# Kernel optimization log

Hardware: AMD Instinct MI355X
Metric: run time of the kernel (lower is better)

## Reference

```python
import jax, jax.numpy as jnp
import numpy as np
from jax import lax

H = 64            # GRU hidden size
NUM_LAYERS = 4
EPS = 1e-5        # BatchNorm eps
NEG_SLOPE = 0.1   # LeakyReLU slope


def setup_inputs() -> dict:
    key = jax.random.key(0)
    ks = jax.random.split(key, 24)
    B, T, D = 4096, 34, 180

    def u(k, shape, fan):
        s = 1.0 / np.sqrt(fan)
        return jax.random.uniform(k, shape, jnp.float32, -s, s)

    inp = {
        "poses": jax.random.normal(ks[0], (B, T, D), jnp.float32),
        # pre_conv: Conv1d(180,16,3) -> BN(16) -> Conv1d(16,8,3) -> BN(8) -> Conv1d(8,8,3)
        "conv1_w": u(ks[1], (16, D, 3), D * 3),
        "conv1_b": u(ks[2], (16,), D * 3),
        "bn1_g": jnp.ones((16,), jnp.float32),
        "bn1_b": jnp.zeros((16,), jnp.float32),
        "conv2_w": u(ks[3], (8, 16, 3), 16 * 3),
        "conv2_b": u(ks[4], (8,), 16 * 3),
        "bn2_g": jnp.ones((8,), jnp.float32),
        "bn2_b": jnp.zeros((8,), jnp.float32),
        "conv3_w": u(ks[5], (8, 8, 3), 8 * 3),
        "conv3_b": u(ks[6], (8,), 8 * 3),
        # GRU layer 0: input 8 -> hidden 64
        "gru0_w_ih": u(ks[7], (3 * H, 8), H),
        # GRU layers 1..3: input 64 -> hidden 64 (stacked)
        "gru_w_ih": u(ks[8], (NUM_LAYERS - 1, 3 * H, H), H),
        "gru_w_hh": u(ks[9], (NUM_LAYERS, 3 * H, H), H),
        "gru_b_ih": u(ks[10], (NUM_LAYERS, 3 * H), H),
        "gru_b_hh": u(ks[11], (NUM_LAYERS, 3 * H), H),
        "out_w": u(ks[12], (1, H), H),
        "out_b": u(ks[13], (1,), H),
        "out2_w": u(ks[14], (1, T - 6), T - 6),
        "out2_b": u(ks[15], (1,), T - 6),
    }
    return inp


def _conv1d(x, w, b):
    # x: [B, C_in, L], w: [C_out, C_in, K] -> [B, C_out, L-K+1]
    y = lax.conv_general_dilated(x, w, (1,), 'VALID',
                                 dimension_numbers=('NCH', 'OIH', 'NCH'))
    return y + b[None, :, None]


def _bn_train(x, g, b):
    # training-mode BatchNorm1d over (batch, length) per channel; x: [B, C, L]
    m = jnp.mean(x, axis=(0, 2), keepdims=True)
    v = jnp.mean(jnp.square(x - m), axis=(0, 2), keepdims=True)  # biased var
    return (x - m) * jax.lax.rsqrt(v + EPS) * g[None, :, None] + b[None, :, None]


def _leaky(x):
    return jnp.where(x >= 0, x, NEG_SLOPE * x)


def _gru_layer(x_tbh, w_ih, w_hh, b_ih, b_hh):
    # x_tbh: [T, B, D_in]; returns outputs [T, B, H]
    xg = jnp.einsum('tbi,gi->tbg', x_tbh, w_ih) + b_ih  # [T, B, 3H]

    def step(h, xg_t):
        hg = h @ w_hh.T + b_hh
        i_r, i_z, i_n = jnp.split(xg_t, 3, axis=-1)
        h_r, h_z, h_n = jnp.split(hg, 3, axis=-1)
        r = jax.nn.sigmoid(i_r + h_r)
        z = jax.nn.sigmoid(i_z + h_z)
        n = jnp.tanh(i_n + r * h_n)
        h_new = n - n * z + z * h  # == (1-z)*n + z*h
        return h_new, h_new

    B = x_tbh.shape[1]
    h0 = jnp.zeros((B, H), x_tbh.dtype)
    _, ys = lax.scan(step, h0, xg)
    return ys


def reference(poses, conv1_w, conv1_b, bn1_g, bn1_b, conv2_w, conv2_b,
              bn2_g, bn2_b, conv3_w, conv3_b, gru0_w_ih, gru_w_ih,
              gru_w_hh, gru_b_ih, gru_b_hh, out_w, out_b, out2_w, out2_b):
    x = jnp.transpose(poses, (0, 2, 1))          # [B, D, T]
    x = _leaky(_bn_train(_conv1d(x, conv1_w, conv1_b), bn1_g, bn1_b))
    x = _leaky(_bn_train(_conv1d(x, conv2_w, conv2_b), bn2_g, bn2_b))
    x = _conv1d(x, conv3_w, conv3_b)             # [B, 8, T-6]
    feat = jnp.transpose(x, (2, 0, 1))           # [T', B, 8] time-major

    out = _gru_layer(feat, gru0_w_ih, gru_w_hh[0], gru_b_ih[0], gru_b_hh[0])
    for i in range(1, NUM_LAYERS):
        out = _gru_layer(out, gru_w_ih[i - 1], gru_w_hh[i], gru_b_ih[i], gru_b_hh[i])

    out = jnp.transpose(out, (1, 0, 2))          # [B, T', H]
    y = jnp.einsum('bth,oh->bto', out, out_w)[..., 0] + out_b[0]  # [B, T']
    y = y @ out2_w[0] + out2_b[0]                # [B]
    return jax.nn.sigmoid(y)[:, None]            # [B, 1]
```

## Files before the change

kernel.cpp:

```cpp
#include <hip/hip_runtime.h>

typedef unsigned short u16;
typedef __attribute__((ext_vector_type(8))) short bf16x8;
typedef __attribute__((ext_vector_type(4))) short bf16x4;
typedef __attribute__((ext_vector_type(4))) float f32x4;

#define TP 28
#define NB 4096
#define L2E 1.4426950408889634f

__device__ __forceinline__ u16 f2bf(float x) {
  union { float f; unsigned u; } v; v.f = x;
  unsigned u = v.u;
  return (u16)((u + 0x7fffu + ((u >> 16) & 1u)) >> 16);
}
__device__ __forceinline__ float bf2f(u16 h) {
  union { unsigned u; float f; } v; v.u = ((unsigned)h) << 16; return v.f;
}
__device__ __forceinline__ float rcp_(float x) {
  float r;
  asm("v_rcp_f32 %0, %1" : "=v"(r) : "v"(x));
  return r;
}
__device__ __forceinline__ float exp2_(float x) {
  float r;
  asm("v_exp_f32 %0, %1" : "=v"(r) : "v"(x));
  return r;
}
__device__ __forceinline__ float sigm2(float x) { return rcp_(1.0f + exp2_(-x)); }
__device__ __forceinline__ float tanh2(float x) { return 1.0f - 2.0f * rcp_(1.0f + exp2_(x)); }
__device__ __forceinline__ float sigm(float x) { return rcp_(1.0f + __expf(-x)); }
__device__ __forceinline__ float leaky(float x) { return x >= 0.0f ? x : 0.1f * x; }
__device__ __forceinline__ f32x4 mfma16(bf16x8 a, bf16x8 b, f32x4 c) {
  return __builtin_amdgcn_mfma_f32_16x16x32_bf16(a, b, c, 0, 0, 0);
}
__device__ __forceinline__ bf16x8 pack8s(float4 a, float4 b, float s) {
  bf16x8 f;
  f[0] = (short)f2bf(a.x * s); f[1] = (short)f2bf(a.y * s);
  f[2] = (short)f2bf(a.z * s); f[3] = (short)f2bf(a.w * s);
  f[4] = (short)f2bf(b.x * s); f[5] = (short)f2bf(b.y * s);
  f[6] = (short)f2bf(b.z * s); f[7] = (short)f2bf(b.w * s);
  return f;
}
__device__ __forceinline__ bf16x8 ldfrag8s(const float* p, float s) {
  float4 u0 = *(const float4*)p;
  float4 u1 = *(const float4*)(p + 4);
  return pack8s(u0, u1, s);
}

__global__ __launch_bounds__(512, 4) void k_conv1(
    const float* __restrict__ poses, const float* __restrict__ w1,
    const float* __restrict__ b1, float* __restrict__ y1,
    float* __restrict__ p1)
{
  __shared__ __align__(16) u16 xw[8][3264];
  __shared__ __align__(16) u16 wt[16][544];
  __shared__ float sp[8][16];
  __shared__ float sq[8][16];
  const int tid = threadIdx.x;
  const int lane = tid & 63;
  const int wv = tid >> 6;

  if (tid < 64) wt[tid >> 2][540 + (tid & 3)] = 0;
  for (int i = tid; i < 8640; i += 512) {
    int co_ = i / 540, r = i % 540, ci = r / 3, tap = r % 3;
    wt[co_][tap * 180 + ci] = f2bf(w1[i]);
  }
  __syncthreads();

  const int b0 = blockIdx.x * 4;
  const int bb = wv >> 1;
  const int b = b0 + bb;
  const int t0 = (wv & 1) * 16;
  {
    const float4* src = (const float4*)(poses + (size_t)b * 6120 + t0 * 180);
    u16* dst = xw[wv];
    if (lane < 24) dst[3240 + lane] = 0;
#pragma unroll
    for (int j = 0; j < 13; ++j) {
      const int idx = j * 64 + lane;
      if (idx < 810) {
        float4 v = src[idx];
        unsigned lo = (unsigned)f2bf(v.x) | ((unsigned)f2bf(v.y) << 16);
        unsigned hi = (unsigned)f2bf(v.z) | ((unsigned)f2bf(v.w) << 16);
        *(uint2*)&dst[idx * 4] = make_uint2(lo, hi);
      }
    }
  }

  const int co = lane & 15;
  const int kgrp = lane >> 4;
  const int kg = kgrp * 8;
  const int R0 = kgrp * 4;
  const u16* pr = &xw[wv][co * 180];
  const float bias = b1[co];
  f32x4 acc = {bias, bias, bias, bias};

#pragma unroll
  for (int s = 0; s < 17; ++s) {
    bf16x4 lo = *(const bf16x4*)(pr + s * 32 + kg);
    bf16x4 hi = *(const bf16x4*)(pr + s * 32 + kg + 4);
    bf16x8 a0 = {lo[0], lo[1], lo[2], lo[3], hi[0], hi[1], hi[2], hi[3]};
    bf16x8 wf = *(const bf16x8*)&wt[co][s * 32 + kg];
    acc = mfma16(a0, wf, acc);
  }

  float s_ = 0.f, q_ = 0.f;
#pragma unroll
  for (int r = 0; r < 4; ++r) { s_ += acc[r]; q_ += acc[r] * acc[r]; }
  *(float4*)(y1 + (size_t)b * 512 + co * 32 + t0 + R0) =
      make_float4(acc[0], acc[1], acc[2], acc[3]);
  s_ += __shfl_xor(s_, 16); q_ += __shfl_xor(q_, 16);
  s_ += __shfl_xor(s_, 32); q_ += __shfl_xor(q_, 32);
  if (lane < 16) { sp[wv][co] = s_; sq[wv][co] = q_; }
  __syncthreads();
  if (tid < 32) {
    int ss = tid >> 4, c = tid & 15;
    float v = 0.f;
#pragma unroll
    for (int w2 = 0; w2 < 8; ++w2) v += ss ? sq[w2][c] : sp[w2][c];
    p1[blockIdx.x * 32 + ss * 16 + c] = v;
  }
}

__global__ __launch_bounds__(1024) void k_stats1(
    const float* __restrict__ p1, const float* __restrict__ g,
    const float* __restrict__ bb, float* __restrict__ sc)
{
  __shared__ float red[32][32];
  __shared__ float tot[32];
  const int tid = threadIdx.x;
  const int col = tid & 31, rg = tid >> 5;
  float a = 0;
  for (int r = rg; r < 1024; r += 32) a += p1[r * 32 + col];
  red[rg][col] = a;
  __syncthreads();
  if (tid < 32) {
    float t = 0;
    for (int i = 0; i < 32; ++i) t += red[i][tid];
    tot[tid] = t;
  }
  __syncthreads();
  if (tid < 16) {
    const float inv = 1.0f / 131072.0f;
    float m = tot[tid] * inv;
    float var = tot[16 + tid] * inv - m * m;
    float s = g[tid] * rsqrtf(fmaxf(var, 0.0f) + 1e-5f);
    sc[tid] = s;
    sc[16 + tid] = bb[tid] - m * s;
  }
}

__global__ __launch_bounds__(256) void k_conv2(
    const float* __restrict__ y1, const float* __restrict__ sc,
    const float* __restrict__ w2, const float* __restrict__ b2,
    float* __restrict__ y2, float* __restrict__ p2)
{
  __shared__ float a1[8][16][33];
  __shared__ float w2s[384];
  __shared__ float sp[4][8][2];
  const int tid = threadIdx.x;
  const int b0 = blockIdx.x * 8;
  for (int i = tid; i < 384; i += 256) w2s[i] = w2[i];
  for (int i = tid; i < 4096; i += 256) {
    int bb = i >> 9, c = (i >> 5) & 15, t = i & 31;
    float v = y1[(size_t)(b0 + bb) * 512 + c * 32 + t] * sc[c] + sc[16 + c];
    a1[bb][c][t] = leaky(v);
  }
  __syncthreads();
  float acc[8];
  const int bb = tid / 30, t = tid % 30;
  const bool act = tid < 240;
#pragma unroll
  for (int co = 0; co < 8; ++co) acc[co] = act ? b2[co] : 0.0f;
  if (act) {
    for (int ci = 0; ci < 16; ++ci) {
      float x0 = a1[bb][ci][t], x1 = a1[bb][ci][t + 1], x2 = a1[bb][ci][t + 2];
#pragma unroll
      for (int co = 0; co < 8; ++co) {
        const float* wp = &w2s[co * 48 + ci * 3];
        acc[co] += x0 * wp[0] + x1 * wp[1] + x2 * wp[2];
      }
    }
    for (int co = 0; co < 8; ++co)
      y2[(size_t)(b0 + bb) * 240 + co * 30 + t] = acc[co];
  }
  const int w = tid >> 6;
#pragma unroll
  for (int co = 0; co < 8; ++co) {
    float s = act ? acc[co] : 0.0f;
    float q = s * s;
#pragma unroll
    for (int m = 1; m <= 32; m <<= 1) { s += __shfl_xor(s, m); q += __shfl_xor(q, m); }
    if ((tid & 63) == 0) { sp[w][co][0] = s; sp[w][co][1] = q; }
  }
  __syncthreads();
  if (tid < 16) {
    int s = tid >> 3, c = tid & 7;
    p2[blockIdx.x * 16 + s * 8 + c] = sp[0][c][s] + sp[1][c][s] + sp[2][c][s] + sp[3][c][s];
  }
}

__global__ __launch_bounds__(256) void k_stats2(
    const float* __restrict__ p2, const float* __restrict__ g,
    const float* __restrict__ bb, float* __restrict__ sc)
{
  __shared__ float red[16][16];
  __shared__ float tot[16];
  const int tid = threadIdx.x;
  const int col = tid & 15, r0 = tid >> 4;
  float a = 0;
  for (int r = r0; r < 512; r += 16) a += p2[r * 16 + col];
  red[r0][col] = a;
  __syncthreads();
  if (tid < 16) {
    float t = 0;
    for (int i = 0; i < 16; ++i) t += red[i][tid];
    tot[tid] = t;
  }
  __syncthreads();
  if (tid < 8) {
    const float inv = 1.0f / 122880.0f;
    float m = tot[tid] * inv;
    float var = tot[8 + tid] * inv - m * m;
    float s = g[tid] * rsqrtf(fmaxf(var, 0.0f) + 1e-5f);
    sc[32 + tid] = s;
    sc[40 + tid] = bb[tid] - m * s;
  }
}

__global__ __launch_bounds__(256) void k_conv3(
    const float* __restrict__ y2, const float* __restrict__ sc,
    const float* __restrict__ w3, const float* __restrict__ b3,
    u16* __restrict__ feat)
{
  __shared__ float a2[8][8][31];
  __shared__ float w3s[192];
  const int tid = threadIdx.x;
  const int b0 = blockIdx.x * 8;
  for (int i = tid; i < 192; i += 256) w3s[i] = w3[i];
  for (int i = tid; i < 1920; i += 256) {
    int bb = i / 240, rem = i % 240, c = rem / 30, t = rem % 30;
    float v = y2[(size_t)(b0 + bb) * 240 + c * 30 + t] * sc[32 + c] + sc[40 + c];
    a2[bb][c][t] = leaky(v);
  }
  __syncthreads();
  if (tid < 224) {
    int bb = tid / 28, t = tid % 28;
    float acc[8];
#pragma unroll
    for (int co = 0; co < 8; ++co) acc[co] = b3[co];
    for (int ci = 0; ci < 8; ++ci) {
      float x0 = a2[bb][ci][t], x1 = a2[bb][ci][t + 1], x2 = a2[bb][ci][t + 2];
#pragma unroll
      for (int co = 0; co < 8; ++co) {
        const float* wp = &w3s[co * 24 + ci * 3];
        acc[co] += x0 * wp[0] + x1 * wp[1] + x2 * wp[2];
      }
    }
    union { u16 h[8]; uint4 v; } u;
#pragma unroll
    for (int co = 0; co < 8; ++co) u.h[co] = f2bf(acc[co]);
    *(uint4*)&feat[((size_t)t * NB + b0 + bb) * 8] = u.v;
  }
}

__global__ __launch_bounds__(1024) void k_gru_pipe(
    const u16* __restrict__ feat,
    const float* __restrict__ g0wih,
    const float* __restrict__ gwih,
    const float* __restrict__ gwhh,
    const float* __restrict__ gbih,
    const float* __restrict__ gbhh,
    const float* __restrict__ ow, const float* __restrict__ ob,
    const float* __restrict__ o2w, const float* __restrict__ o2b,
    float* __restrict__ out)
{
  __shared__ __align__(16) u16 xl[2][16][40];
  __shared__ __align__(16) u16 hl[4][2][16][72];
  __shared__ float sph[4][16];
  const int tid = threadIdx.x;
  const int b0 = blockIdx.x * 16;
  const int lane = tid & 63;
  const int wv = tid >> 6;
  const int l = wv >> 2;
  const int c = wv & 3;
  const int row = lane & 15;
  const int kgrp = lane >> 4;
  const int kg = kgrp * 8;
  const int R0 = kgrp * 4;
  const int cr = c * 16 + row;

  for (int i = tid; i < 4 * 2 * 16 * 72; i += 1024) ((u16*)hl)[i] = 0;
  for (int i = tid; i < 2 * 16 * 40; i += 1024) ((u16*)xl)[i] = 0;

  bf16x8 Wx[3][2], Wh[3][2];
  if (l == 0) {
#pragma unroll
    for (int g = 0; g < 3; ++g) {
      const float sc_ = (g == 2) ? 2.f * L2E : L2E;
      bf16x8 z;
#pragma unroll
      for (int j = 0; j < 8; ++j) z[j] = 0;
      if (kg == 0) z = ldfrag8s(g0wih + (g * 64 + cr) * 8, sc_);
      Wx[g][0] = z;
      Wx[g][1] = z;
    }
  } else {
#pragma unroll
    for (int g = 0; g < 3; ++g) {
      const float sc_ = (g == 2) ? 2.f * L2E : L2E;
#pragma unroll
      for (int s = 0; s < 2; ++s)
        Wx[g][s] = ldfrag8s(gwih + (l - 1) * 12288 + (g * 64 + cr) * 64 + s * 32 + kg, sc_);
    }
  }
#pragma unroll
  for (int g = 0; g < 3; ++g) {
    const float sc_ = (g == 2) ? 2.f * L2E : L2E;
#pragma unroll
    for (int s = 0; s < 2; ++s)
      Wh[g][s] = ldfrag8s(gwhh + l * 12288 + (g * 64 + cr) * 64 + s * 32 + kg, sc_);
  }

  const float br = (gbih[l * 192 + cr] + gbhh[l * 192 + cr]) * L2E;
  const float bz = (gbih[l * 192 + 64 + cr] + gbhh[l * 192 + 64 + cr]) * L2E;
  const float bi = gbih[l * 192 + 128 + cr] * 2.f * L2E;
  const float bh = gbhh[l * 192 + 128 + cr] * 2.f * L2E;

  float hold[4] = {0.f, 0.f, 0.f, 0.f};
  float accL[4] = {0.f, 0.f, 0.f, 0.f};
  const float owv = ow[cr];

  uint2 pf = make_uint2(0u, 0u);
  const bool xldr = (wv == 0 && lane < 32);
  if (xldr)
    pf = *(const uint2*)(feat + ((size_t)0 * NB + b0 + (lane >> 1)) * 8 + (lane & 1) * 4);
  __syncthreads();
  if (xldr)
    *(uint2*)&xl[0][lane >> 1][(lane & 1) * 4] = pf;
  __syncthreads();

  for (int tick = 0; tick < TP + 3; ++tick) {
    const int t = tick - l;
    if (t >= 0 && t < TP) {
      const int cur = t & 1, nxt = cur ^ 1;
      bf16x8 ax0, ax1, ah0, ah1;
      if (l == 0) {
        ax0 = *(const bf16x8*)&xl[cur][row][kg];
      } else {
        ax0 = *(const bf16x8*)&hl[l - 1][nxt][row][kg];
        ax1 = *(const bf16x8*)&hl[l - 1][nxt][row][32 + kg];
      }
      ah0 = *(const bf16x8*)&hl[l][cur][row][kg];
      ah1 = *(const bf16x8*)&hl[l][cur][row][32 + kg];
      if (xldr && t + 1 < TP)
        pf = *(const uint2*)(feat + ((size_t)(t + 1) * NB + b0 + (lane >> 1)) * 8 + (lane & 1) * 4);

      f32x4 ar = {br, br, br, br};
      f32x4 az = {bz, bz, bz, bz};
      f32x4 ai = {bi, bi, bi, bi};
      f32x4 an = {bh, bh, bh, bh};

      __builtin_amdgcn_s_setprio(1);
      ar = mfma16(ax0, Wx[0][0], ar);
      az = mfma16(ax0, Wx[1][0], az);
      ai = mfma16(ax0, Wx[2][0], ai);
      if (l != 0) {
        ar = mfma16(ax1, Wx[0][1], ar);
        az = mfma16(ax1, Wx[1][1], az);
        ai = mfma16(ax1, Wx[2][1], ai);
      }
      ar = mfma16(ah0, Wh[0][0], ar);
      ar = mfma16(ah1, Wh[0][1], ar);
      az = mfma16(ah0, Wh[1][0], az);
      az = mfma16(ah1, Wh[1][1], az);
      an = mfma16(ah0, Wh[2][0], an);
      an = mfma16(ah1, Wh[2][1], an);
      __builtin_amdgcn_s_setprio(0);

      float o2 = 0.f;
      if (l == 3) o2 = o2w[t];
      u16 hb[4];
#pragma unroll
      for (int r = 0; r < 4; ++r) {
        float rr = sigm2(ar[r]);
        float zz = sigm2(az[r]);
        float nn = tanh2(ai[r] + rr * an[r]);
        float hv = nn + zz * (hold[r] - nn);
        hold[r] = hv;
        hb[r] = f2bf(hv);
        if (l == 3) accL[r] += hv * owv * o2;
      }
#pragma unroll
      for (int r = 0; r < 4; ++r) hl[l][nxt][R0 + r][cr] = hb[r];
      if (xldr && t + 1 < TP)
        *(uint2*)&xl[(t + 1) & 1][lane >> 1][(lane & 1) * 4] = pf;
    }
    __syncthreads();
  }

  if (l == 3) {
#pragma unroll
    for (int r = 0; r < 4; ++r) {
      accL[r] += __shfl_xor(accL[r], 1);
      accL[r] += __shfl_xor(accL[r], 2);
      accL[r] += __shfl_xor(accL[r], 4);
      accL[r] += __shfl_xor(accL[r], 8);
    }
    if ((lane & 15) == 0) {
#pragma unroll
      for (int r = 0; r < 4; ++r) sph[c][R0 + r] = accL[r];
    }
  }
  __syncthreads();
  if (tid < 16) {
    float s = sph[0][tid] + sph[1][tid] + sph[2][tid] + sph[3][tid];
    float so2 = 0.f;
    for (int t = 0; t < TP; ++t) so2 += o2w[t];
    out[b0 + tid] = sigm(s + ob[0] * so2 + o2b[0]);
  }
}

extern "C" void kernel_launch(void* const* d_in, const int* in_sizes, int n_in,
                              void* d_out, int out_size, void* d_ws, size_t ws_size,
                              hipStream_t stream)
{
  const float* poses = (const float*)d_in[0];
  const float* c1w = (const float*)d_in[1];
  const float* c1b = (const float*)d_in[2];
  const float* bn1g = (const float*)d_in[3];
  const float* bn1b = (const float*)d_in[4];
  const float* c2w = (const float*)d_in[5];
  const float* c2b = (const float*)d_in[6];
  const float* bn2g = (const float*)d_in[7];
  const float* bn2b = (const float*)d_in[8];
  const float* c3w = (const float*)d_in[9];
  const float* c3b = (const float*)d_in[10];
  const float* g0wih = (const float*)d_in[11];
  const float* gwih = (const float*)d_in[12];
  const float* gwhh = (const float*)d_in[13];
  const float* gbih = (const float*)d_in[14];
  const float* gbhh = (const float*)d_in[15];
  const float* ow = (const float*)d_in[16];
  const float* ob = (const float*)d_in[17];
  const float* o2w = (const float*)d_in[18];
  const float* o2b = (const float*)d_in[19];

  float* ws = (float*)d_ws;
  float* y1 = ws;
  float* y2 = ws + 2097152;
  u16* feat = (u16*)(ws + 3080192);
  float* p1 = ws + 3538944;
  float* p2 = ws + 3604480;
  float* sc = ws + 3612672;
  float* outv = (float*)d_out;

  k_conv1<<<dim3(1024), dim3(512), 0, stream>>>(poses, c1w, c1b, y1, p1);
  k_stats1<<<dim3(1), dim3(1024), 0, stream>>>(p1, bn1g, bn1b, sc);
  k_conv2<<<dim3(512), dim3(256), 0, stream>>>(y1, sc, c2w, c2b, y2, p2);
  k_stats2<<<dim3(1), dim3(256), 0, stream>>>(p2, bn2g, bn2b, sc);
  k_conv3<<<dim3(512), dim3(256), 0, stream>>>(y2, sc, c3w, c3b, feat);
  k_gru_pipe<<<dim3(256), dim3(1024), 0, stream>>>(feat, g0wih, gwih, gwhh,
                                                   gbih, gbhh, ow, ob, o2w, o2b, outv);
}
```

Before: 110.7 us.

## Fuse BN stats into conv kernels via last-block reduction and conv3 into GRU

Removes the two single-block BN statistics kernels by having the last block of conv1 and conv2 (detected with an atomic counter) do the final reduction and write the scale and shift. Conv3 now runs inside the GRU kernel: each block computes its 16 batch rows' features into shared memory for all timesteps, which replaces the global feat buffer and the per-step prefetch. This saves three launches and a global round trip, at the cost of a memset, more shared memory in the GRU kernel and a serial tail in the last block of each conv kernel.

Result: slower. 309.7 us (+179.7%).

```diff
diff --git a/kernel.cpp b/kernel.cpp
--- a/kernel.cpp
+++ b/kernel.cpp
@@ -13,9 +13,6 @@
   union { float f; unsigned u; } v; v.f = x;
   unsigned u = v.u;
   return (u16)((u + 0x7fffu + ((u >> 16) & 1u)) >> 16);
-}
-__device__ __forceinline__ float bf2f(u16 h) {
-  union { unsigned u; float f; } v; v.u = ((unsigned)h) << 16; return v.f;
 }
 __device__ __forceinline__ float rcp_(float x) {
   float r;
@@ -50,13 +47,18 @@
 
 __global__ __launch_bounds__(512, 4) void k_conv1(
     const float* __restrict__ poses, const float* __restrict__ w1,
-    const float* __restrict__ b1, float* __restrict__ y1,
-    float* __restrict__ p1)
+    const float* __restrict__ b1, const float* __restrict__ bn1g,
+    const float* __restrict__ bn1b, float* __restrict__ y1,
+    float* __restrict__ p1, float* __restrict__ sc,
+    unsigned* __restrict__ cnt)
 {
   __shared__ __align__(16) u16 xw[8][3264];
   __shared__ __align__(16) u16 wt[16][544];
   __shared__ float sp[8][16];
   __shared__ float sq[8][16];
+  __shared__ float redl[16][32];
+  __shared__ float totl[32];
+  __shared__ int lastFlag;
   const int tid = threadIdx.x;
   const int lane = tid & 63;
   const int wv = tid >> 6;
@@ -121,44 +123,48 @@
     for (int w2 = 0; w2 < 8; ++w2) v += ss ? sq[w2][c] : sp[w2][c];
     p1[blockIdx.x * 32 + ss * 16 + c] = v;
   }
-}
-
-__global__ __launch_bounds__(1024) void k_stats1(
-    const float* __restrict__ p1, const float* __restrict__ g,
-    const float* __restrict__ bb, float* __restrict__ sc)
-{
-  __shared__ float red[32][32];
-  __shared__ float tot[32];
-  const int tid = threadIdx.x;
-  const int col = tid & 31, rg = tid >> 5;
-  float a = 0;
-  for (int r = rg; r < 1024; r += 32) a += p1[r * 32 + col];
-  red[rg][col] = a;
-  __syncthreads();
-  if (tid < 32) {
-    float t = 0;
-    for (int i = 0; i < 32; ++i) t += red[i][tid];
-    tot[tid] = t;
-  }
-  __syncthreads();
-  if (tid < 16) {
-    const float inv = 1.0f / 131072.0f;
-    float m = tot[tid] * inv;
-    float var = tot[16 + tid] * inv - m * m;
-    float s = g[tid] * rsqrtf(fmaxf(var, 0.0f) + 1e-5f);
-    sc[tid] = s;
-    sc[16 + tid] = bb[tid] - m * s;
+  __threadfence();
+  __syncthreads();
+  if (tid == 0) lastFlag = (atomicAdd(cnt, 1u) == 1023u) ? 1 : 0;
+  __syncthreads();
+  if (lastFlag) {
+    __threadfence();
+    const int col = tid & 31, rg = tid >> 5;
+    float a = 0;
+    for (int r = rg; r < 1024; r += 16) a += p1[r * 32 + col];
+    redl[rg][col] = a;
+    __syncthreads();
+    if (tid < 32) {
+      float t = 0;
+#pragma unroll
+      for (int i = 0; i < 16; ++i) t += redl[i][tid];
+      totl[tid] = t;
+    }
+    __syncthreads();
+    if (tid < 16) {
+      const float inv = 1.0f / 131072.0f;
+      float m = totl[tid] * inv;
+      float var = totl[16 + tid] * inv - m * m;
+      float s = bn1g[tid] * rsqrtf(fmaxf(var, 0.0f) + 1e-5f);
+      sc[tid] = s;
+      sc[16 + tid] = bn1b[tid] - m * s;
+    }
   }
 }
 
 __global__ __launch_bounds__(256) void k_conv2(
     const float* __restrict__ y1, const float* __restrict__ sc,
     const float* __restrict__ w2, const float* __restrict__ b2,
-    float* __restrict__ y2, float* __restrict__ p2)
+    const float* __restrict__ bn2g, const float* __restrict__ bn2b,
+    float* __restrict__ y2, float* __restrict__ p2,
+    float* __restrict__ scw, unsigned* __restrict__ cnt)
 {
   __shared__ float a1[8][16][33];
   __shared__ float w2s[384];
   __shared__ float sp[4][8][2];
+  __shared__ float redl[16][16];
+  __shared__ float totl[16];
+  __shared__ int lastFlag;
   const int tid = threadIdx.x;
   const int b0 = blockIdx.x * 8;
   for (int i = tid; i < 384; i += 256) w2s[i] = w2[i];
@@ -199,74 +205,38 @@
     int s = tid >> 3, c = tid & 7;
     p2[blockIdx.x * 16 + s * 8 + c] = sp[0][c][s] + sp[1][c][s] + sp[2][c][s] + sp[3][c][s];
   }
-}
-
-__global__ __launch_bounds__(256) void k_stats2(
-    const float* __restrict__ p2, const float* __restrict__ g,
-    const float* __restrict__ bb, float* __restrict__ sc)
-{
-  __shared__ float red[16][16];
-  __shared__ float tot[16];
-  const int tid = threadIdx.x;
-  const int col = tid & 15, r0 = tid >> 4;
-  float a = 0;
-  for (int r = r0; r < 512; r += 16) a += p2[r * 16 + col];
-  red[r0][col] = a;
-  __syncthreads();
-  if (tid < 16) {
-    float t = 0;
-    for (int i = 0; i < 16; ++i) t += red[i][tid];
-    tot[tid] = t;
-  }
-  __syncthreads();
-  if (tid < 8) {
-    const float inv = 1.0f / 122880.0f;
-    float m = tot[tid] * inv;
-    float var = tot[8 + tid] * inv - m * m;
-    float s = g[tid] * rsqrtf(fmaxf(var, 0.0f) + 1e-5f);
-    sc[32 + tid] = s;
-    sc[40 + tid] = bb[tid] - m * s;
-  }
-}
-
-__global__ __launch_bounds__(256) void k_conv3(
+  __threadfence();
+  __syncthreads();
+  if (tid == 0) lastFlag = (atomicAdd(cnt, 1u) == 511u) ? 1 : 0;
+  __syncthreads();
+  if (lastFlag) {
+    __threadfence();
+    const int col = tid & 15, rg = tid >> 4;
+    float a = 0;
+    for (int r = rg; r < 512; r += 16) a += p2[r * 16 + col];
+    redl[rg][col] = a;
+    __syncthreads();
+    if (tid < 16) {
+      float tt = 0;
+#pragma unroll
+      for (int i = 0; i < 16; ++i) tt += redl[i][tid];
+      totl[tid] = tt;
+    }
+    __syncthreads();
+    if (tid < 8) {
+      const float inv = 1.0f / 122880.0f;
+      float m = totl[tid] * inv;
+      float var = totl[8 + tid] * inv - m * m;
+      float s = bn2g[tid] * rsqrtf(fmaxf(var, 0.0f) + 1e-5f);
+      scw[32 + tid] = s;
+      scw[40 + tid] = bn2b[tid] - m * s;
+    }
+  }
+}
+
+__global__ __launch_bounds__(1024) void k_gru_pipe(
     const float* __restrict__ y2, const float* __restrict__ sc,
     const float* __restrict__ w3, const float* __restrict__ b3,
-    u16* __restrict__ feat)
-{
-  __shared__ float a2[8][8][31];
-  __shared__ float w3s[192];
-  const int tid = threadIdx.x;
-  const int b0 = blockIdx.x * 8;
-  for (int i = tid; i < 192; i += 256) w3s[i] = w3[i];
-  for (int i = tid; i < 1920; i += 256) {
-    int bb = i / 240, rem = i % 240, c = rem / 30, t = rem % 30;
-    float v = y2[(size_t)(b0 + bb) * 240 + c * 30 + t] * sc[32 + c] + sc[40 + c];
-    a2[bb][c][t] = leaky(v);
-  }
-  __syncthreads();
-  if (tid < 224) {
-    int bb = tid / 28, t = tid % 28;
-    float acc[8];
-#pragma unroll
-    for (int co = 0; co < 8; ++co) acc[co] = b3[co];
-    for (int ci = 0; ci < 8; ++ci) {
-      float x0 = a2[bb][ci][t], x1 = a2[bb][ci][t + 1], x2 = a2[bb][ci][t + 2];
-#pragma unroll
-      for (int co = 0; co < 8; ++co) {
-        const float* wp = &w3s[co * 24 + ci * 3];
-        acc[co] += x0 * wp[0] + x1 * wp[1] + x2 * wp[2];
-      }
-    }
-    union { u16 h[8]; uint4 v; } u;
-#pragma unroll
-    for (int co = 0; co < 8; ++co) u.h[co] = f2bf(acc[co]);
-    *(uint4*)&feat[((size_t)t * NB + b0 + bb) * 8] = u.v;
-  }
-}
-
-__global__ __launch_bounds__(1024) void k_gru_pipe(
-    const u16* __restrict__ feat,
     const float* __restrict__ g0wih,
     const float* __restrict__ gwih,
     const float* __restrict__ gwhh,
@@ -276,8 +246,10 @@
     const float* __restrict__ o2w, const float* __restrict__ o2b,
     float* __restrict__ out)
 {
-  __shared__ __align__(16) u16 xl[2][16][40];
+  __shared__ __align__(16) u16 featl[TP][16][40];
   __shared__ __align__(16) u16 hl[4][2][16][72];
+  __shared__ float a2[16][8][31];
+  __shared__ float w3s[192];
   __shared__ float sph[4][16];
   const int tid = threadIdx.x;
   const int b0 = blockIdx.x * 16;
@@ -292,7 +264,13 @@
   const int cr = c * 16 + row;
 
   for (int i = tid; i < 4 * 2 * 16 * 72; i += 1024) ((u16*)hl)[i] = 0;
-  for (int i = tid; i < 2 * 16 * 40; i += 1024) ((u16*)xl)[i] = 0;
+  for (int i = tid; i < TP * 16 * 40; i += 1024) ((u16*)featl)[i] = 0;
+  for (int i = tid; i < 192; i += 1024) w3s[i] = w3[i];
+  for (int i = tid; i < 3840; i += 1024) {
+    int bb = i / 240, rem = i % 240, cc = rem / 30, tt = rem % 30;
+    float v = y2[(size_t)(b0 + bb) * 240 + cc * 30 + tt] * sc[32 + cc] + sc[40 + cc];
+    a2[bb][cc][tt] = leaky(v);
+  }
 
   bf16x8 Wx[3][2], Wh[3][2];
   if (l == 0) {
@@ -328,18 +306,31 @@
   const float bi = gbih[l * 192 + 128 + cr] * 2.f * L2E;
   const float bh = gbhh[l * 192 + 128 + cr] * 2.f * L2E;
 
+  __syncthreads();
+
+  if (tid < 448) {
+    int bb = tid / 28, t = tid % 28;
+    float accc[8];
+#pragma unroll
+    for (int co = 0; co < 8; ++co) accc[co] = b3[co];
+    for (int ci = 0; ci < 8; ++ci) {
+      float x0 = a2[bb][ci][t], x1 = a2[bb][ci][t + 1], x2 = a2[bb][ci][t + 2];
+#pragma unroll
+      for (int co = 0; co < 8; ++co) {
+        const float* wp = &w3s[co * 24 + ci * 3];
+        accc[co] += x0 * wp[0] + x1 * wp[1] + x2 * wp[2];
+      }
+    }
+    union { u16 h[8]; uint4 v; } u;
+#pragma unroll
+    for (int co = 0; co < 8; ++co) u.h[co] = f2bf(accc[co]);
+    *(uint4*)&featl[t][bb][0] = u.v;
+  }
+  __syncthreads();
+
   float hold[4] = {0.f, 0.f, 0.f, 0.f};
   float accL[4] = {0.f, 0.f, 0.f, 0.f};
   const float owv = ow[cr];
-
-  uint2 pf = make_uint2(0u, 0u);
-  const bool xldr = (wv == 0 && lane < 32);
-  if (xldr)
-    pf = *(const uint2*)(feat + ((size_t)0 * NB + b0 + (lane >> 1)) * 8 + (lane & 1) * 4);
-  __syncthreads();
-  if (xldr)
-    *(uint2*)&xl[0][lane >> 1][(lane & 1) * 4] = pf;
-  __syncthreads();
 
   for (int tick = 0; tick < TP + 3; ++tick) {
     const int t = tick - l;
@@ -347,15 +338,13 @@
       const int cur = t & 1, nxt = cur ^ 1;
       bf16x8 ax0, ax1, ah0, ah1;
       if (l == 0) {
-        ax0 = *(const bf16x8*)&xl[cur][row][kg];
+        ax0 = *(const bf16x8*)&featl[t][row][kg];
       } else {
         ax0 = *(const bf16x8*)&hl[l - 1][nxt][row][kg];
         ax1 = *(const bf16x8*)&hl[l - 1][nxt][row][32 + kg];
       }
       ah0 = *(const bf16x8*)&hl[l][cur][row][kg];
       ah1 = *(const bf16x8*)&hl[l][cur][row][32 + kg];
-      if (xldr && t + 1 < TP)
-        pf = *(const uint2*)(feat + ((size_t)(t + 1) * NB + b0 + (lane >> 1)) * 8 + (lane & 1) * 4);
 
       f32x4 ar = {br, br, br, br};
       f32x4 az = {bz, bz, bz, bz};
@@ -394,8 +383,6 @@
       }
 #pragma unroll
       for (int r = 0; r < 4; ++r) hl[l][nxt][R0 + r][cr] = hb[r];
-      if (xldr && t + 1 < TP)
-        *(uint2*)&xl[(t + 1) & 1][lane >> 1][(lane & 1) * 4] = pf;
     }
     __syncthreads();
   }
@@ -450,17 +437,18 @@
   float* ws = (float*)d_ws;
   float* y1 = ws;
   float* y2 = ws + 2097152;
-  u16* feat = (u16*)(ws + 3080192);
-  float* p1 = ws + 3538944;
-  float* p2 = ws + 3604480;
-  float* sc = ws + 3612672;
+  float* p1 = ws + 3080192;
+  float* p2 = ws + 3112960;
+  float* sc = ws + 3121152;
+  unsigned* cnt = (unsigned*)(ws + 3121200);
   float* outv = (float*)d_out;
 
-  k_conv1<<<dim3(1024), dim3(512), 0, stream>>>(poses, c1w, c1b, y1, p1);
-  k_stats1<<<dim3(1), dim3(1024), 0, stream>>>(p1, bn1g, bn1b, sc);
-  k_conv2<<<dim3(512), dim3(256), 0, stream>>>(y1, sc, c2w, c2b, y2, p2);
-  k_stats2<<<dim3(1), dim3(256), 0, stream>>>(p2, bn2g, bn2b, sc);
-  k_conv3<<<dim3(512), dim3(256), 0, stream>>>(y2, sc, c3w, c3b, feat);
-  k_gru_pipe<<<dim3(256), dim3(1024), 0, stream>>>(feat, g0wih, gwih, gwhh,
-                                                   gbih, gbhh, ow, ob, o2w, o2b, outv);
-}
+  hipMemsetAsync(cnt, 0, 8, stream);
+  k_conv1<<<dim3(1024), dim3(512), 0, stream>>>(poses, c1w, c1b, bn1g, bn1b,
+                                                y1, p1, sc, cnt);
+  k_conv2<<<dim3(512), dim3(256), 0, stream>>>(y1, sc, c2w, c2b, bn2g, bn2b,
+                                               y2, p2, sc, cnt + 1);
+  k_gru_pipe<<<dim3(256), dim3(1024), 0, stream>>>(y2, sc, c3w, c3b,
+                                                   g0wih, gwih, gwhh, gbih, gbhh,
+                                                   ow, ob, o2w, o2b, outv);
+}
```
